# Performance work log

Measured on AMD Instinct MI355X. Metric: run time of the kernel, lower is better.

Reference implementation:

```python
import jax, jax.numpy as jnp
import numpy as np

FG_THR = 0.7
BG_THR = 0.3
NUM_PER_IMAGE = 256
NUM_POS_MAX = int(NUM_PER_IMAGE * 0.5)  # positive_ratio = 0.5
BBOX_W = (1.0, 1.0, 1.0, 1.0)
BETA = 1.0 / 9.0


def _permute(t, C):
    # N x (A*C) x H x W -> N x (H*W*A) x C, matching RPNLoss.permute
    N, _, H, W = t.shape
    t = t.reshape(N, -1, C, H, W)
    t = jnp.transpose(t, (0, 3, 4, 1, 2))
    return t.reshape(N, -1, C)


def _iou(a, b):
    # a: [N,4], b: [M,4] -> [N,M] (with +1 box convention, as in source)
    x_tl = jnp.maximum(a[:, None, 0], b[None, :, 0])
    y_tl = jnp.maximum(a[:, None, 1], b[None, :, 1])
    x_rb = jnp.minimum(a[:, None, 2], b[None, :, 2])
    y_rb = jnp.minimum(a[:, None, 3], b[None, :, 3])
    inter = jnp.clip(x_rb - x_tl + 1.0, 0.0) * jnp.clip(y_rb - y_tl + 1.0, 0.0)
    area1 = (a[:, 2] - a[:, 0] + 1.0) * (a[:, 3] - a[:, 1] + 1.0)
    area2 = (b[:, 2] - b[:, 0] + 1.0) * (b[:, 3] - b[:, 1] + 1.0)
    return inter / (area1[:, None] + area2[None, :] - inter)


def _encode(anchors, targets):
    ws = anchors[:, 2] - anchors[:, 0] + 1.0
    hs = anchors[:, 3] - anchors[:, 1] + 1.0
    x_ctr = anchors[:, 0] + 0.5 * ws
    y_ctr = anchors[:, 1] + 0.5 * hs
    t_ws = targets[:, 2] - targets[:, 0] + 1.0
    t_hs = targets[:, 3] - targets[:, 1] + 1.0
    t_x = targets[:, 0] + 0.5 * t_ws
    t_y = targets[:, 1] + 0.5 * t_hs
    wx, wy, ww, wh = BBOX_W
    tx = wx * (t_x - x_ctr) / ws
    ty = wy * (t_y - y_ctr) / hs
    tw = ww * jnp.log(t_ws / ws)
    th = wh * jnp.log(t_hs / hs)
    return jnp.stack([tx, ty, tw, th], axis=1)


def _bce_logits(l, t):
    return jnp.maximum(l, 0.0) - l * t + jnp.log1p(jnp.exp(-jnp.abs(l)))


def _per_image(anchor, logit, breg, size, target, key):
    N = anchor.shape[0]
    ious = _iou(anchor, target)  # [N, M]
    vals = ious.max(axis=1)
    ori = jnp.argmax(ious, axis=1).astype(jnp.int32)
    inds = jnp.where(vals < BG_THR, -1, ori)
    inds = jnp.where((vals >= BG_THR) & (vals < FG_THR), -2, inds)
    # low-quality matches: anchors achieving the per-target max IoU keep their argmax
    col_max = ious.max(axis=0)
    restore = (ious == col_max[None, :]).any(axis=1)
    inds = jnp.where(restore, ori, inds)
    # filter_anchors: keep anchors fully inside the image (size = (h, w))
    inside = (anchor[:, 0] >= 0) & (anchor[:, 1] >= 0) & \
             (anchor[:, 2] <= size[1] - 1.0) & (anchor[:, 3] <= size[0] - 1.0)
    inds = jnp.where(inside, inds, -2)

    pos = inds >= 0
    neg = inds == -1
    # random sampling via random priorities + fixed-size top_k with validity masks
    r = jax.random.uniform(key, (N,))
    pos_vals, pos_idx = jax.lax.top_k(jnp.where(pos, r, -1.0), NUM_POS_MAX)
    valid_pos = pos_vals >= 0.0
    num_pos = valid_pos.sum()
    neg_vals, neg_idx = jax.lax.top_k(jnp.where(neg, r, -1.0), NUM_PER_IMAGE)
    valid_neg = (neg_vals >= 0.0) & (jnp.arange(NUM_PER_IMAGE) < (NUM_PER_IMAGE - num_pos))

    # classification loss terms (BCE with logits); pos target 1, neg target 0
    vp = valid_pos.astype(logit.dtype)
    vn = valid_neg.astype(logit.dtype)
    cls_sum = jnp.sum(_bce_logits(logit[pos_idx], 1.0) * vp) + \
              jnp.sum(_bce_logits(logit[neg_idx], 0.0) * vn)
    count = num_pos + valid_neg.sum()

    m = jnp.clip(inds[pos_idx], 0, None)
    offsets = _encode(anchor[pos_idx], target[m])
    diff = jnp.abs(breg[pos_idx] - offsets)
    sl1 = jnp.where(diff < BETA, 0.5 * diff * diff / BETA, diff - 0.5 * BETA)
    reg_sum = jnp.sum(sl1 * vp[:, None])
    return cls_sum, count, reg_sum


def reference(anchors, logits, bbox_regs, sizes, targets):
    B = anchors.shape[0]
    log = _permute(logits, 1)[..., 0]      # [B, H*W*A]
    breg = _permute(bbox_regs, 4)          # [B, H*W*A, 4]
    keys = jax.random.split(jax.random.key(42), B)
    cls_s, cnt, reg_s = jax.vmap(_per_image)(anchors, log, breg, sizes, targets, keys)
    total = jnp.sum(cnt).astype(anchors.dtype)
    cls_loss = jnp.sum(cls_s) / total
    reg_loss = jnp.sum(reg_s) / total
    return jnp.stack([cls_loss, reg_loss])


def setup_inputs() -> dict:
    key = jax.random.key(0)
    ks = jax.random.split(key, 10)
    B, A, H, W, M = 4, 3, 168, 256, 32
    N = H * W * A
    IMG_H, IMG_W = 800.0, 1333.0
    x1 = jax.random.uniform(ks[0], (B, N)) * 1200.0
    y1 = jax.random.uniform(ks[1], (B, N)) * 700.0
    aw = jax.random.uniform(ks[2], (B, N)) * 300.0 + 16.0
    ah = jax.random.uniform(ks[3], (B, N)) * 300.0 + 16.0
    anchors = jnp.stack([x1, y1, x1 + aw, y1 + ah], axis=-1)  # some out of image -> filtered
    tx1 = jax.random.uniform(ks[4], (B, M)) * 1000.0
    ty1 = jax.random.uniform(ks[5], (B, M)) * 500.0
    tw = jax.random.uniform(ks[6], (B, M)) * 250.0 + 30.0
    th = jax.random.uniform(ks[7], (B, M)) * 200.0 + 30.0
    targets = jnp.stack([tx1, ty1, jnp.minimum(tx1 + tw, IMG_W - 1.0),
                         jnp.minimum(ty1 + th, IMG_H - 1.0)], axis=-1)
    logits = jax.random.normal(ks[8], (B, A, H, W), dtype=jnp.float32)
    bbox_regs = jax.random.normal(ks[9], (B, 4 * A, H, W), dtype=jnp.float32) * 0.1
    sizes = jnp.tile(jnp.array([IMG_H, IMG_W], dtype=jnp.float32), (B, 1))
    return {"anchors": anchors, "logits": logits, "bbox_regs": bbox_regs,
            "sizes": sizes, "targets": targets}
```

## Files before the change

### kernel.cpp

```cpp
#include <hip/hip_runtime.h>
#include <stdint.h>

#define Bn 4
#define An 3
#define Hn 168
#define Wn 256
#define Mn 32
#define HWn (Hn*Wn)
#define Nn (HWn*An)
#define POS_CAP 8192
#define NPERIM 256
#define NPOSMAX 128
#define FG_THR 0.7f
#define BG_THR 0.3f
#define BETA (1.0f/9.0f)

#define NBLK 504
#define APT 1
#define NWAVES (NBLK * 4)
#define BUCKET_CAP 256
#define TSEG_CAP 64

#define OFF_POSCNT 0
#define OFF_COUNT  8
#define OFF_CLS    9
#define OFF_REG    10
#define OFF_DONE   11
#define OFF_BINCNT 16
#define OFF_BINBCE 4112
#define ZERO_WORDS 8208
#define OFF_PCM    8208
#define OFF_WPCM   72720
#define OFF_TSEGC  330768
#define OFF_PLIST  338832
#define OFF_BUCKET 404368
#define OFF_TSEG   2501520

__device__ __forceinline__ uint32_t rotl32(uint32_t v, int n) { return (v << n) | (v >> (32 - n)); }

__device__ __forceinline__ void tf2x32(uint32_t k0, uint32_t k1, uint32_t x0, uint32_t x1,
                                       uint32_t& o0, uint32_t& o1) {
    uint32_t k2 = k0 ^ k1 ^ 0x1BD11BDAu;
    x0 += k0; x1 += k1;
    x0 += x1; x1 = rotl32(x1, 13); x1 ^= x0;
    x0 += x1; x1 = rotl32(x1, 15); x1 ^= x0;
    x0 += x1; x1 = rotl32(x1, 26); x1 ^= x0;
    x0 += x1; x1 = rotl32(x1, 6);  x1 ^= x0;
    x0 += k1; x1 += k2 + 1u;
    x0 += x1; x1 = rotl32(x1, 17); x1 ^= x0;
    x0 += x1; x1 = rotl32(x1, 29); x1 ^= x0;
    x0 += x1; x1 = rotl32(x1, 16); x1 ^= x0;
    x0 += x1; x1 = rotl32(x1, 24); x1 ^= x0;
    x0 += k2; x1 += k0 + 2u;
    x0 += x1; x1 = rotl32(x1, 13); x1 ^= x0;
    x0 += x1; x1 = rotl32(x1, 15); x1 ^= x0;
    x0 += x1; x1 = rotl32(x1, 26); x1 ^= x0;
    x0 += x1; x1 = rotl32(x1, 6);  x1 ^= x0;
    x0 += k0; x1 += k1 + 3u;
    x0 += x1; x1 = rotl32(x1, 17); x1 ^= x0;
    x0 += x1; x1 = rotl32(x1, 29); x1 ^= x0;
    x0 += x1; x1 = rotl32(x1, 16); x1 ^= x0;
    x0 += x1; x1 = rotl32(x1, 24); x1 ^= x0;
    x0 += k1; x1 += k2 + 4u;
    x0 += x1; x1 = rotl32(x1, 13); x1 ^= x0;
    x0 += x1; x1 = rotl32(x1, 15); x1 ^= x0;
    x0 += x1; x1 = rotl32(x1, 26); x1 ^= x0;
    x0 += x1; x1 = rotl32(x1, 6);  x1 ^= x0;
    x0 += k2; x1 += k0 + 5u;
    o0 = x0; o1 = x1;
}

__device__ __forceinline__ uint32_t rng_m23(uint32_t k0, uint32_t k1, uint32_t i) {
    uint32_t o0, o1;
    tf2x32(k0, k1, 0u, i, o0, o1);
    return (o0 ^ o1) >> 9;
}

__device__ __forceinline__ uint32_t vload(const uint32_t* p) {
    return *(const volatile uint32_t*)p;
}

__device__ __forceinline__ float iou_one(float a0, float a1, float a2, float a3,
                                         float t0, float t1, float t2, float t3) {
    float xtl = fmaxf(a0, t0), ytl = fmaxf(a1, t1);
    float xrb = fminf(a2, t2), yrb = fminf(a3, t3);
    float iw = fmaxf(xrb - xtl + 1.0f, 0.0f);
    float ih = fmaxf(yrb - ytl + 1.0f, 0.0f);
    float inter = iw * ih;
    float area1 = (a2 - a0 + 1.0f) * (a3 - a1 + 1.0f);
    float area2 = (t2 - t0 + 1.0f) * (t3 - t1 + 1.0f);
    return inter * __builtin_amdgcn_rcpf(area1 + area2 - inter);
}

__device__ __forceinline__ float bce0(float l) {
    return fmaxf(l, 0.0f) + log1pf(expf(-fabsf(l)));
}

__device__ __forceinline__ bool sel_less(uint2 a, uint2 b) {
    return (a.x > b.x) || (a.x == b.x && a.y < b.y);
}

__device__ void bitonic_sort_shared(uint2* buf, int n) {
    for (int k = 2; k <= n; k <<= 1) {
        for (int j = k >> 1; j > 0; j >>= 1) {
            for (int t = (int)threadIdx.x; t < n; t += (int)blockDim.x) {
                int ixj = t ^ j;
                if (ixj > t) {
                    uint2 x = buf[t], y = buf[ixj];
                    bool up = ((t & k) == 0);
                    bool sw = up ? sel_less(y, x) : sel_less(x, y);
                    if (sw) { buf[t] = y; buf[ixj] = x; }
                }
            }
            __syncthreads();
        }
    }
}

__global__ void __launch_bounds__(256) k0_init(uint32_t* __restrict__ ws) {
    int i = blockIdx.x * 256 + (int)threadIdx.x;
    if (i < ZERO_WORDS) ws[i] = 0u;
}

__global__ void __launch_bounds__(256) k1_iou(const float* __restrict__ anchors,
                                              const float* __restrict__ targets,
                                              const float* __restrict__ sizes,
                                              const float* __restrict__ logits,
                                              uint32_t* __restrict__ ws) {
    const int b = blockIdx.y, j = blockIdx.x, tid = threadIdx.x;
    const int wid = tid >> 6, lane = tid & 63;
    __shared__ float part[4][Mn];

    uint32_t key0, key1;
    tf2x32(0u, 42u, 0u, (uint32_t)b, key0, key1);

    const int i = j * 256 + tid;
    float4 av = ((const float4*)anchors)[b * Nn + i];

    float rowmax = -1.0f; int ori = 0; uint32_t tie = 0u;
    float mycm = 0.0f;
    #pragma unroll 4
    for (int t = 0; t < Mn; ++t) {
        float4 tv = ((const float4*)targets)[b * Mn + t];
        float io = iou_one(av.x, av.y, av.z, av.w, tv.x, tv.y, tv.z, tv.w);
        if (io > rowmax) { rowmax = io; ori = t; }
        float m0 = io;
        #pragma unroll
        for (int o = 32; o > 0; o >>= 1) m0 = fmaxf(m0, __shfl_xor(m0, o, 64));
        if (lane == t) mycm = m0;
        tie |= (io == m0) ? (1u << t) : 0u;
    }

    const int wimg = j * 4 + wid;
    if (lane < Mn) {
        ws[OFF_WPCM + ((size_t)b * NWAVES + wimg) * 32 + lane] = __float_as_uint(mycm);
        part[wid][lane] = mycm;
    }
    __syncthreads();
    if (tid < Mn) {
        float v = fmaxf(fmaxf(part[0][tid], part[1][tid]),
                        fmaxf(part[2][tid], part[3][tid]));
        ws[OFF_PCM + ((size_t)b * NBLK + j) * Mn + tid] = __float_as_uint(v);
    }

    const float sh = sizes[b * 2 + 0], sw = sizes[b * 2 + 1];
    unsigned long long lt_mask = (lane == 63) ? 0x7FFFFFFFFFFFFFFFull
                                              : ((1ull << lane) - 1ull);
    bool inside = (av.x >= 0.0f) && (av.y >= 0.0f) &&
                  (av.z <= sw - 1.0f) && (av.w <= sh - 1.0f);
    bool fg = rowmax >= FG_THR;
    bool bg = rowmax < BG_THR;
    bool posn   = inside && fg;
    bool defern = inside && !fg && (tie != 0u);
    bool negn   = inside && bg && (tie == 0u);
    uint32_t m = rng_m23(key0, key1, (uint32_t)i);

    const int a_ = i % An, hw_ = i / An;
    float lneg = 0.0f;
    if (negn) lneg = logits[(b * An + a_) * HWn + hw_];

    unsigned long long pmask = __ballot(posn);
    if (pmask) {
        int leader = __ffsll((long long)pmask) - 1;
        uint32_t bb = 0;
        if (lane == leader) bb = atomicAdd(&ws[OFF_POSCNT + b], (uint32_t)__popcll(pmask));
        bb = __shfl(bb, leader, 64);
        if (posn) {
            uint32_t p = bb + (uint32_t)__popcll(pmask & lt_mask);
            if (p < POS_CAP)
                ((uint2*)(ws + OFF_PLIST))[(size_t)b * POS_CAP + p] =
                    make_uint2(m, (uint32_t)i | ((uint32_t)ori << 17));
        }
    }
    unsigned long long dmask = __ballot(defern);
    if (defern) {
        uint32_t slot = (uint32_t)__popcll(dmask & lt_mask);
        ((uint4*)(ws + OFF_TSEG))[((size_t)b * NWAVES + wimg) * TSEG_CAP + slot] =
            make_uint4(tie, m,
                       (uint32_t)i | ((uint32_t)ori << 17) | (bg ? (1u << 22) : 0u),
                       0u);
    }
    if (lane == 0) ws[OFF_TSEGC + b * NWAVES + wimg] = (uint32_t)__popcll(dmask);
    if (negn) {
        int bin = (int)(m >> 13);
        uint32_t slot = atomicAdd(&ws[OFF_BINCNT + (b << 10) + bin], 1u);
        if (slot < BUCKET_CAP)
            ((uint2*)(ws + OFF_BUCKET))[((((size_t)b << 10) + bin) << 8) + slot] =
                make_uint2(m, (uint32_t)i);
        atomicAdd((float*)&ws[OFF_BINBCE + (b << 10) + bin], bce0(lneg));
    }
}

__global__ void __launch_bounds__(256) k2_resolve(const float* __restrict__ logits,
                                                  uint32_t* __restrict__ ws) {
    const int b = blockIdx.y, j = blockIdx.x, tid = threadIdx.x;
    const int lane = tid & 63;
    __shared__ float redf[256];
    __shared__ uint32_t cmb[Mn];
    __shared__ uint32_t eqs[4];
    __shared__ uint32_t cnts[4];

    {
        int t = tid & 31, sub = tid >> 5;
        float acc = 0.0f;
        for (int jj = sub; jj < NBLK; jj += 8)
            acc = fmaxf(acc, __uint_as_float(ws[OFF_PCM + ((size_t)b * NBLK + jj) * Mn + t]));
        redf[tid] = acc;
        __syncthreads();
        if (sub == 0) {
            #pragma unroll
            for (int q = 1; q < 8; ++q) acc = fmaxf(acc, redf[t + 32 * q]);
            cmb[t] = __float_as_uint(acc);
        }
    }
    if (tid < 4) {
        eqs[tid] = 0u;
        cnts[tid] = ws[OFF_TSEGC + b * NWAVES + j * 4 + tid];
    }
    __syncthreads();
    if (tid < 128) {
        int lw = tid >> 5, t2 = tid & 31;
        uint32_t wv = ws[OFF_WPCM + ((size_t)b * NWAVES + j * 4 + lw) * 32 + t2];
        if (wv == cmb[t2]) atomicOr(&eqs[lw], 1u << t2);
    }
    __syncthreads();

    const uint32_t c0 = cnts[0], c1 = cnts[1], c2 = cnts[2], c3 = cnts[3];
    const int total = (int)(c0 + c1 + c2 + c3);
    unsigned long long lt_mask = (lane == 63) ? 0x7FFFFFFFFFFFFFFFull
                                              : ((1ull << lane) - 1ull);
    for (int f = tid; f < total; f += 256) {
        int lw, o;
        if ((uint32_t)f < c0)                { lw = 0; o = f; }
        else if ((uint32_t)f < c0 + c1)      { lw = 1; o = f - (int)c0; }
        else if ((uint32_t)f < c0 + c1 + c2) { lw = 2; o = f - (int)(c0 + c1); }
        else                                 { lw = 3; o = f - (int)(c0 + c1 + c2); }
        uint4 e = ((const uint4*)(ws + OFF_TSEG))
                      [((size_t)b * NWAVES + j * 4 + lw) * TSEG_CAP + o];
        int i = (int)(e.z & 0x1FFFFu);
        bool restored = (e.x & eqs[lw]) != 0u;

        unsigned long long rmask = __ballot(restored);
        if (rmask) {
            int leader = __ffsll((long long)rmask) - 1;
            uint32_t bb = 0;
            if (lane == leader) bb = atomicAdd(&ws[OFF_POSCNT + b], (uint32_t)__popcll(rmask));
            bb = __shfl(bb, leader, 64);
            if (restored) {
                uint32_t p = bb + (uint32_t)__popcll(rmask & lt_mask);
                if (p < POS_CAP)
                    ((uint2*)(ws + OFF_PLIST))[(size_t)b * POS_CAP + p] =
                        make_uint2(e.y, e.z & 0x3FFFFFu);
            }
        }
        if (!restored && (e.z & (1u << 22))) {
            uint32_t m = e.y;
            int bin = (int)(m >> 13);
            uint32_t slot = atomicAdd(&ws[OFF_BINCNT + (b << 10) + bin], 1u);
            if (slot < BUCKET_CAP)
                ((uint2*)(ws + OFF_BUCKET))[((((size_t)b << 10) + bin) << 8) + slot] =
                    make_uint2(m, (uint32_t)i);
            int a = i % An, hw = i / An;
            float l = logits[(b * An + a) * HWn + hw];
            atomicAdd((float*)&ws[OFF_BINBCE + (b << 10) + bin], bce0(l));
        }
    }
}

__global__ void __launch_bounds__(1024) k3_final(const float* __restrict__ anchors,
                                                 const float* __restrict__ targets,
                                                 const float* __restrict__ logits,
                                                 const float* __restrict__ bregs,
                                                 uint32_t* __restrict__ ws,
                                                 float* __restrict__ out) {
    const int b = blockIdx.x, tid = threadIdx.x;
    __shared__ uint32_t csum[1024];
    __shared__ uint2 buf[2048];
    __shared__ float fred[1024];
    __shared__ int s_bd, s_need;
    float cls = 0.0f, reg = 0.0f;

    csum[tid] = vload(ws + OFF_BINCNT + (b << 10) + tid);
    __syncthreads();
    for (int off = 1; off < 1024; off <<= 1) {
        uint32_t v = csum[tid];
        uint32_t add = (tid + off < 1024) ? csum[tid + off] : 0u;
        __syncthreads();
        csum[tid] = v + add;
        __syncthreads();
    }
    uint32_t pc = vload(ws + OFF_POSCNT + b);
    int num_pos = (pc < (uint32_t)NPOSMAX) ? (int)pc : NPOSMAX;
    int k_neg = NPERIM - num_pos;
    uint32_t total = csum[0];
    if (tid == 0 && (int)total < k_neg) { s_bd = -1; s_need = 0; }
    {
        uint32_t inclv = csum[tid];
        uint32_t nxt = (tid < 1023) ? csum[tid + 1] : 0u;
        if ((int)total >= k_neg && (int)inclv >= k_neg && (int)nxt < k_neg) {
            s_bd = tid; s_need = k_neg - (int)nxt;
        }
    }
    if (tid == 0) {
        int sel_negs = ((int)total < k_neg) ? (int)total : k_neg;
        atomicAdd(&ws[OFF_COUNT], (uint32_t)(num_pos + sel_negs));
    }
    __syncthreads();
    const int bd = s_bd, need = s_need;
    if ((int)tid > bd)
        cls += __uint_as_float(vload(ws + OFF_BINBCE + (b << 10) + tid));
    __syncthreads();

    if (need > 0) {
        int cnt = (int)vload(ws + OFF_BINCNT + (b << 10) + bd);
        if (cnt > BUCKET_CAP) cnt = BUCKET_CAP;
        const uint2* bkt = (const uint2*)(ws + OFF_BUCKET) + ((((size_t)b << 10) + bd) << 8);
        for (int t = tid; t < cnt; t += 1024) buf[t] = bkt[t];
        int npad = 1; while (npad < cnt) npad <<= 1;
        for (int t = tid; t < npad; t += 1024) if (t >= cnt) buf[t] = make_uint2(0u, 0xFFFFFFFFu);
        __syncthreads();
        bitonic_sort_shared(buf, npad);
        int sel = (need < cnt) ? need : cnt;
        for (int t = tid; t < sel; t += 1024) {
            int i = (int)buf[t].y;
            int a = i % An, hw = i / An;
            float l = logits[(b * An + a) * HWn + hw];
            cls += bce0(l);
        }
    }
    __syncthreads();

    {
        int pci = (pc < (uint32_t)POS_CAP) ? (int)pc : POS_CAP;
        const uint2* plist = (const uint2*)(ws + OFF_PLIST) + (size_t)b * POS_CAP;
        int psel = (pci < NPOSMAX) ? pci : NPOSMAX;
        bool use_buf = false;
        if (pci > NPOSMAX) {
            int n = (pci < 2048) ? pci : 2048;
            for (int t = tid; t < n; t += 1024) buf[t] = plist[t];
            int npad = 1; while (npad < n) npad <<= 1;
            for (int t = tid; t < npad; t += 1024) if (t >= n) buf[t] = make_uint2(0u, 0xFFFFFFFFu);
            __syncthreads();
            bitonic_sort_shared(buf, npad);
            use_buf = true;
            psel = (NPOSMAX < n) ? NPOSMAX : n;
        }
        for (int t = tid; t < psel; t += 1024) {
            uint32_t packed = use_buf ? buf[t].y : plist[t].y;
            int i = (int)(packed & 0x1FFFFu);
            int orit = (int)((packed >> 17) & 0x1Fu);
            int a = i % An, hw = i / An;
            float l = logits[(b * An + a) * HWn + hw];
            cls += fmaxf(l, 0.0f) - l + log1pf(expf(-fabsf(l)));
            float4 avx = ((const float4*)anchors)[b * Nn + i];
            float4 tv = ((const float4*)targets)[b * Mn + orit];
            float aws = avx.z - avx.x + 1.0f, ahs = avx.w - avx.y + 1.0f;
            float axc = avx.x + 0.5f * aws, ayc = avx.y + 0.5f * ahs;
            float tws = tv.z - tv.x + 1.0f, ths = tv.w - tv.y + 1.0f;
            float txc = tv.x + 0.5f * tws, tyc = tv.y + 0.5f * ths;
            float off0 = (txc - axc) / aws;
            float off1 = (tyc - ayc) / ahs;
            float off2 = logf(tws / aws);
            float off3 = logf(ths / ahs);
            float br0 = bregs[(b * 12 + a * 4 + 0) * HWn + hw];
            float br1 = bregs[(b * 12 + a * 4 + 1) * HWn + hw];
            float br2 = bregs[(b * 12 + a * 4 + 2) * HWn + hw];
            float br3 = bregs[(b * 12 + a * 4 + 3) * HWn + hw];
            float d;
            d = fabsf(br0 - off0); reg += (d < BETA) ? 0.5f * d * d / BETA : d - 0.5f * BETA;
            d = fabsf(br1 - off1); reg += (d < BETA) ? 0.5f * d * d / BETA : d - 0.5f * BETA;
            d = fabsf(br2 - off2); reg += (d < BETA) ? 0.5f * d * d / BETA : d - 0.5f * BETA;
            d = fabsf(br3 - off3); reg += (d < BETA) ? 0.5f * d * d / BETA : d - 0.5f * BETA;
        }
    }

    fred[tid] = cls;
    __syncthreads();
    for (int s = 512; s > 0; s >>= 1) {
        if (tid < s) fred[tid] += fred[tid + s];
        __syncthreads();
    }
    if (tid == 0 && fred[0] != 0.0f) atomicAdd((float*)&ws[OFF_CLS], fred[0]);
    __syncthreads();
    fred[tid] = reg;
    __syncthreads();
    for (int s = 512; s > 0; s >>= 1) {
        if (tid < s) fred[tid] += fred[tid + s];
        __syncthreads();
    }
    if (tid == 0) {
        if (fred[0] != 0.0f) atomicAdd((float*)&ws[OFF_REG], fred[0]);
        __threadfence();
        uint32_t old = atomicAdd(&ws[OFF_DONE], 1u);
        if (old == Bn - 1) {
            float cls_tot = __uint_as_float(atomicAdd(&ws[OFF_CLS], 0u));
            float reg_tot = __uint_as_float(atomicAdd(&ws[OFF_REG], 0u));
            float cnt = (float)atomicAdd(&ws[OFF_COUNT], 0u);
            out[0] = cls_tot / cnt;
            out[1] = reg_tot / cnt;
        }
    }
}

extern "C" void kernel_launch(void* const* d_in, const int* in_sizes, int n_in,
                              void* d_out, int out_size, void* d_ws, size_t ws_size,
                              hipStream_t stream) {
    const float* anchors = (const float*)d_in[0];
    const float* logits  = (const float*)d_in[1];
    const float* bregs   = (const float*)d_in[2];
    const float* sizes   = (const float*)d_in[3];
    const float* targets = (const float*)d_in[4];
    float* out = (float*)d_out;
    uint32_t* ws = (uint32_t*)d_ws;

    k0_init<<<dim3((ZERO_WORDS + 255) / 256), dim3(256), 0, stream>>>(ws);
    k1_iou<<<dim3(NBLK, Bn), dim3(256), 0, stream>>>(anchors, targets, sizes, logits, ws);
    k2_resolve<<<dim3(NBLK, Bn), dim3(256), 0, stream>>>(logits, ws);
    k3_final<<<dim3(Bn), dim3(1024), 0, stream>>>(anchors, targets, logits, bregs, ws, out);
}
```

Baseline: 190.2 us.

## Fuse final selection into resolve kernel via last-block pattern and per-wave negative segments

The final per-image selection kernel is merged into the resolve kernel: the last block to finish for each image, detected with an atomic counter, does the histogram scan, boundary-bin gather, sorts and loss sums. Negative candidates are now written to per-wave segments, and only high-score bins keep global buckets. Other boundary bins are rebuilt by scanning all segments in the finishing block. This removes one kernel launch and most per-negative bucket scatter writes. The cost is a possibly long serial scan over thousands of segments when the boundary bin is cold, and the tail work runs on a 256-thread block instead of 1024.

```diff
diff --git a/kernel.cpp b/kernel.cpp
--- a/kernel.cpp
+++ b/kernel.cpp
@@ -16,25 +16,33 @@
 #define BETA (1.0f/9.0f)
 
 #define NBLK 504
-#define APT 1
-#define NWAVES (NBLK * 4)
-#define BUCKET_CAP 256
+#define NWAVES (NBLK*4)
 #define TSEG_CAP 64
+#define NSEG_CAP 64
+#define XSEG_CAP 256
+#define BIN_HOT 960
+#define NHOT 64
+#define HB_CAP 256
 
 #define OFF_POSCNT 0
+#define OFF_DONEI  4
 #define OFF_COUNT  8
 #define OFF_CLS    9
 #define OFF_REG    10
-#define OFF_DONE   11
+#define OFF_DONEA  11
 #define OFF_BINCNT 16
 #define OFF_BINBCE 4112
 #define ZERO_WORDS 8208
 #define OFF_PCM    8208
 #define OFF_WPCM   72720
 #define OFF_TSEGC  330768
-#define OFF_PLIST  338832
-#define OFF_BUCKET 404368
-#define OFF_TSEG   2501520
+#define OFF_NSEGC  338832
+#define OFF_XSEGC  346896
+#define OFF_PLIST  348912
+#define OFF_HBUCK  414448
+#define OFF_TSEG   545520
+#define OFF_NSEG   2609904
+#define OFF_XSEG   3642096
 
 __device__ __forceinline__ uint32_t rotl32(uint32_t v, int n) { return (v << n) | (v >> (32 - n)); }
 
@@ -80,6 +88,11 @@
     return *(const volatile uint32_t*)p;
 }
 
+__device__ __forceinline__ void st64(uint2* p, uint2 v) {
+    atomicExch((unsigned long long*)p,
+               ((unsigned long long)v.y << 32) | (unsigned long long)v.x);
+}
+
 __device__ __forceinline__ float iou_one(float a0, float a1, float a2, float a3,
                                          float t0, float t1, float t2, float t3) {
     float xtl = fmaxf(a0, t0), ytl = fmaxf(a1, t1);
@@ -197,152 +210,231 @@
         uint32_t slot = (uint32_t)__popcll(dmask & lt_mask);
         ((uint4*)(ws + OFF_TSEG))[((size_t)b * NWAVES + wimg) * TSEG_CAP + slot] =
             make_uint4(tie, m,
-                       (uint32_t)i | ((uint32_t)ori << 17) | (bg ? (1u << 22) : 0u),
-                       0u);
-    }
-    if (lane == 0) ws[OFF_TSEGC + b * NWAVES + wimg] = (uint32_t)__popcll(dmask);
+                       (uint32_t)i | ((uint32_t)ori << 17) | (bg ? (1u << 22) : 0u), 0u);
+    }
+    unsigned long long nmask = __ballot(negn);
     if (negn) {
+        uint32_t slot = (uint32_t)__popcll(nmask & lt_mask);
+        ((uint2*)(ws + OFF_NSEG))[((size_t)b * NWAVES + wimg) * NSEG_CAP + slot] =
+            make_uint2(m, (uint32_t)i);
         int bin = (int)(m >> 13);
-        uint32_t slot = atomicAdd(&ws[OFF_BINCNT + (b << 10) + bin], 1u);
-        if (slot < BUCKET_CAP)
-            ((uint2*)(ws + OFF_BUCKET))[((((size_t)b << 10) + bin) << 8) + slot] =
-                make_uint2(m, (uint32_t)i);
+        if (bin >= BIN_HOT) {
+            uint32_t s2 = atomicAdd(&ws[OFF_BINCNT + (b << 10) + bin], 1u);
+            if (s2 < HB_CAP)
+                ((uint2*)(ws + OFF_HBUCK))[((size_t)b * NHOT + (bin - BIN_HOT)) * HB_CAP + s2] =
+                    make_uint2(m, (uint32_t)i);
+        } else {
+            atomicAdd(&ws[OFF_BINCNT + (b << 10) + bin], 1u);
+        }
         atomicAdd((float*)&ws[OFF_BINBCE + (b << 10) + bin], bce0(lneg));
     }
-}
-
-__global__ void __launch_bounds__(256) k2_resolve(const float* __restrict__ logits,
-                                                  uint32_t* __restrict__ ws) {
+    if (lane == 0) {
+        ws[OFF_TSEGC + b * NWAVES + wimg] = (uint32_t)__popcll(dmask);
+        ws[OFF_NSEGC + b * NWAVES + wimg] = (uint32_t)__popcll(nmask);
+    }
+}
+
+__global__ void __launch_bounds__(256) k2_resolve(const float* __restrict__ anchors,
+                                                  const float* __restrict__ targets,
+                                                  const float* __restrict__ logits,
+                                                  const float* __restrict__ bregs,
+                                                  uint32_t* __restrict__ ws,
+                                                  float* __restrict__ out) {
     const int b = blockIdx.y, j = blockIdx.x, tid = threadIdx.x;
     const int lane = tid & 63;
-    __shared__ float redf[256];
     __shared__ uint32_t cmb[Mn];
     __shared__ uint32_t eqs[4];
     __shared__ uint32_t cnts[4];
-
-    {
-        int t = tid & 31, sub = tid >> 5;
-        float acc = 0.0f;
-        for (int jj = sub; jj < NBLK; jj += 8)
-            acc = fmaxf(acc, __uint_as_float(ws[OFF_PCM + ((size_t)b * NBLK + jj) * Mn + t]));
-        redf[tid] = acc;
+    __shared__ uint32_t sx_cnt, s_fcnt;
+    __shared__ int s_last, s_bd, s_need;
+    union U {
+        float part[8][32];
+        struct { uint32_t csum[256]; uint2 buf[2048]; float red[256]; } fin;
+    };
+    __shared__ U u;
+
+    if (tid < 4) { eqs[tid] = 0u; cnts[tid] = ws[OFF_TSEGC + b * NWAVES + j * 4 + tid]; }
+    if (tid == 0) sx_cnt = 0u;
+    __syncthreads();
+    const int total = (int)(cnts[0] + cnts[1] + cnts[2] + cnts[3]);
+
+    if (total > 0) {
+        {
+            float acc = 0.0f;
+            const uint32_t* pcm = ws + OFF_PCM + (size_t)b * NBLK * Mn;
+            for (int w = tid; w < NBLK * Mn; w += 256)
+                acc = fmaxf(acc, __uint_as_float(pcm[w]));
+            u.part[tid >> 5][tid & 31] = acc;
+            __syncthreads();
+            if (tid < Mn) {
+                float v = u.part[0][tid];
+                #pragma unroll
+                for (int q = 1; q < 8; ++q) v = fmaxf(v, u.part[q][tid]);
+                cmb[tid] = __float_as_uint(v);
+            }
+            __syncthreads();
+        }
+        if (tid < 128) {
+            int lw = tid >> 5, t2 = tid & 31;
+            uint32_t wv = ws[OFF_WPCM + ((size_t)b * NWAVES + j * 4 + lw) * 32 + t2];
+            if (wv == cmb[t2]) atomicOr(&eqs[lw], 1u << t2);
+        }
         __syncthreads();
-        if (sub == 0) {
-            #pragma unroll
-            for (int q = 1; q < 8; ++q) acc = fmaxf(acc, redf[t + 32 * q]);
-            cmb[t] = __float_as_uint(acc);
-        }
-    }
-    if (tid < 4) {
-        eqs[tid] = 0u;
-        cnts[tid] = ws[OFF_TSEGC + b * NWAVES + j * 4 + tid];
-    }
-    __syncthreads();
-    if (tid < 128) {
-        int lw = tid >> 5, t2 = tid & 31;
-        uint32_t wv = ws[OFF_WPCM + ((size_t)b * NWAVES + j * 4 + lw) * 32 + t2];
-        if (wv == cmb[t2]) atomicOr(&eqs[lw], 1u << t2);
-    }
-    __syncthreads();
-
-    const uint32_t c0 = cnts[0], c1 = cnts[1], c2 = cnts[2], c3 = cnts[3];
-    const int total = (int)(c0 + c1 + c2 + c3);
-    unsigned long long lt_mask = (lane == 63) ? 0x7FFFFFFFFFFFFFFFull
-                                              : ((1ull << lane) - 1ull);
-    for (int f = tid; f < total; f += 256) {
-        int lw, o;
-        if ((uint32_t)f < c0)                { lw = 0; o = f; }
-        else if ((uint32_t)f < c0 + c1)      { lw = 1; o = f - (int)c0; }
-        else if ((uint32_t)f < c0 + c1 + c2) { lw = 2; o = f - (int)(c0 + c1); }
-        else                                 { lw = 3; o = f - (int)(c0 + c1 + c2); }
-        uint4 e = ((const uint4*)(ws + OFF_TSEG))
-                      [((size_t)b * NWAVES + j * 4 + lw) * TSEG_CAP + o];
-        int i = (int)(e.z & 0x1FFFFu);
-        bool restored = (e.x & eqs[lw]) != 0u;
-
-        unsigned long long rmask = __ballot(restored);
-        if (rmask) {
-            int leader = __ffsll((long long)rmask) - 1;
-            uint32_t bb = 0;
-            if (lane == leader) bb = atomicAdd(&ws[OFF_POSCNT + b], (uint32_t)__popcll(rmask));
-            bb = __shfl(bb, leader, 64);
-            if (restored) {
-                uint32_t p = bb + (uint32_t)__popcll(rmask & lt_mask);
-                if (p < POS_CAP)
-                    ((uint2*)(ws + OFF_PLIST))[(size_t)b * POS_CAP + p] =
-                        make_uint2(e.y, e.z & 0x3FFFFFu);
-            }
-        }
-        if (!restored && (e.z & (1u << 22))) {
-            uint32_t m = e.y;
-            int bin = (int)(m >> 13);
-            uint32_t slot = atomicAdd(&ws[OFF_BINCNT + (b << 10) + bin], 1u);
-            if (slot < BUCKET_CAP)
-                ((uint2*)(ws + OFF_BUCKET))[((((size_t)b << 10) + bin) << 8) + slot] =
-                    make_uint2(m, (uint32_t)i);
-            int a = i % An, hw = i / An;
-            float l = logits[(b * An + a) * HWn + hw];
-            atomicAdd((float*)&ws[OFF_BINBCE + (b << 10) + bin], bce0(l));
-        }
-    }
-}
-
-__global__ void __launch_bounds__(1024) k3_final(const float* __restrict__ anchors,
-                                                 const float* __restrict__ targets,
-                                                 const float* __restrict__ logits,
-                                                 const float* __restrict__ bregs,
-                                                 uint32_t* __restrict__ ws,
-                                                 float* __restrict__ out) {
-    const int b = blockIdx.x, tid = threadIdx.x;
-    __shared__ uint32_t csum[1024];
-    __shared__ uint2 buf[2048];
-    __shared__ float fred[1024];
-    __shared__ int s_bd, s_need;
+
+        const uint32_t c0 = cnts[0], c1 = cnts[1], c2 = cnts[2], c3 = cnts[3];
+        unsigned long long lt_mask = (lane == 63) ? 0x7FFFFFFFFFFFFFFFull
+                                                  : ((1ull << lane) - 1ull);
+        for (int f = tid; f < total; f += 256) {
+            int lw, o;
+            if ((uint32_t)f < c0)                { lw = 0; o = f; }
+            else if ((uint32_t)f < c0 + c1)      { lw = 1; o = f - (int)c0; }
+            else if ((uint32_t)f < c0 + c1 + c2) { lw = 2; o = f - (int)(c0 + c1); }
+            else                                 { lw = 3; o = f - (int)(c0 + c1 + c2); }
+            uint4 e = ((const uint4*)(ws + OFF_TSEG))
+                          [((size_t)b * NWAVES + j * 4 + lw) * TSEG_CAP + o];
+            int i = (int)(e.z & 0x1FFFFu);
+            bool restored = (e.x & eqs[lw]) != 0u;
+
+            unsigned long long rmask = __ballot(restored);
+            if (rmask) {
+                int leader = __ffsll((long long)rmask) - 1;
+                uint32_t bb = 0;
+                if (lane == leader) bb = atomicAdd(&ws[OFF_POSCNT + b], (uint32_t)__popcll(rmask));
+                bb = __shfl(bb, leader, 64);
+                if (restored) {
+                    uint32_t p = bb + (uint32_t)__popcll(rmask & lt_mask);
+                    if (p < POS_CAP)
+                        st64(&((uint2*)(ws + OFF_PLIST))[(size_t)b * POS_CAP + p],
+                             make_uint2(e.y, e.z & 0x3FFFFFu));
+                }
+            }
+            if (!restored && (e.z & (1u << 22))) {
+                uint32_t m = e.y;
+                int bin = (int)(m >> 13);
+                if (bin >= BIN_HOT) {
+                    uint32_t s2 = atomicAdd(&ws[OFF_BINCNT + (b << 10) + bin], 1u);
+                    if (s2 < HB_CAP)
+                        st64(&((uint2*)(ws + OFF_HBUCK))
+                                 [((size_t)b * NHOT + (bin - BIN_HOT)) * HB_CAP + s2],
+                             make_uint2(m, (uint32_t)i));
+                } else {
+                    atomicAdd(&ws[OFF_BINCNT + (b << 10) + bin], 1u);
+                }
+                int a = i % An, hw = i / An;
+                float l = logits[(b * An + a) * HWn + hw];
+                atomicAdd((float*)&ws[OFF_BINBCE + (b << 10) + bin], bce0(l));
+                uint32_t xs = atomicAdd(&sx_cnt, 1u);
+                if (xs < XSEG_CAP)
+                    st64(&((uint2*)(ws + OFF_XSEG))[((size_t)b * NBLK + j) * XSEG_CAP + xs],
+                         make_uint2(m, (uint32_t)i));
+            }
+        }
+    }
+    __syncthreads();
+    if (tid == 0) ws[OFF_XSEGC + b * NBLK + j] = sx_cnt;
+
+    __threadfence();
+    __syncthreads();
+    if (tid == 0) {
+        uint32_t old = atomicAdd(&ws[OFF_DONEI + b], 1u);
+        s_last = (old == (uint32_t)(NBLK - 1)) ? 1 : 0;
+    }
+    __syncthreads();
+    if (!s_last) return;
+
+    __threadfence();
     float cls = 0.0f, reg = 0.0f;
 
-    csum[tid] = vload(ws + OFF_BINCNT + (b << 10) + tid);
-    __syncthreads();
-    for (int off = 1; off < 1024; off <<= 1) {
-        uint32_t v = csum[tid];
-        uint32_t add = (tid + off < 1024) ? csum[tid + off] : 0u;
+    uint32_t c4[4];
+    #pragma unroll
+    for (int q = 0; q < 4; ++q) c4[q] = vload(ws + OFF_BINCNT + (b << 10) + 4 * tid + q);
+    u.fin.csum[tid] = c4[0] + c4[1] + c4[2] + c4[3];
+    __syncthreads();
+    for (int off = 1; off < 256; off <<= 1) {
+        uint32_t mine = u.fin.csum[tid];
+        uint32_t add = (tid + off < 256) ? u.fin.csum[tid + off] : 0u;
         __syncthreads();
-        csum[tid] = v + add;
+        u.fin.csum[tid] = mine + add;
         __syncthreads();
     }
     uint32_t pc = vload(ws + OFF_POSCNT + b);
     int num_pos = (pc < (uint32_t)NPOSMAX) ? (int)pc : NPOSMAX;
     int k_neg = NPERIM - num_pos;
-    uint32_t total = csum[0];
-    if (tid == 0 && (int)total < k_neg) { s_bd = -1; s_need = 0; }
+    uint32_t total_n = u.fin.csum[0];
+    if (tid == 0 && (int)total_n < k_neg) { s_bd = -1; s_need = 0; }
     {
-        uint32_t inclv = csum[tid];
-        uint32_t nxt = (tid < 1023) ? csum[tid + 1] : 0u;
-        if ((int)total >= k_neg && (int)inclv >= k_neg && (int)nxt < k_neg) {
-            s_bd = tid; s_need = k_neg - (int)nxt;
+        uint32_t incl = u.fin.csum[tid];
+        uint32_t nxt = (tid < 255) ? u.fin.csum[tid + 1] : 0u;
+        if ((int)total_n >= k_neg && (int)incl >= k_neg && (int)nxt < k_neg) {
+            int cum = (int)nxt, boundary = -1, needed = 0;
+            #pragma unroll
+            for (int q = 3; q >= 0; --q) {
+                int c = (int)c4[q];
+                if (cum + c >= k_neg) { boundary = 4 * tid + q; needed = k_neg - cum; break; }
+                cum += c;
+            }
+            s_bd = boundary; s_need = needed;
         }
     }
     if (tid == 0) {
-        int sel_negs = ((int)total < k_neg) ? (int)total : k_neg;
+        int sel_negs = ((int)total_n < k_neg) ? (int)total_n : k_neg;
         atomicAdd(&ws[OFF_COUNT], (uint32_t)(num_pos + sel_negs));
     }
     __syncthreads();
     const int bd = s_bd, need = s_need;
-    if ((int)tid > bd)
-        cls += __uint_as_float(vload(ws + OFF_BINBCE + (b << 10) + tid));
+    #pragma unroll
+    for (int q = 0; q < 4; ++q) {
+        int bin = 4 * tid + q;
+        if (bin > bd) cls += __uint_as_float(vload(ws + OFF_BINBCE + (b << 10) + bin));
+    }
     __syncthreads();
 
     if (need > 0) {
-        int cnt = (int)vload(ws + OFF_BINCNT + (b << 10) + bd);
-        if (cnt > BUCKET_CAP) cnt = BUCKET_CAP;
-        const uint2* bkt = (const uint2*)(ws + OFF_BUCKET) + ((((size_t)b << 10) + bd) << 8);
-        for (int t = tid; t < cnt; t += 1024) buf[t] = bkt[t];
+        int cnt;
+        if (bd >= BIN_HOT) {
+            cnt = (int)vload(ws + OFF_BINCNT + (b << 10) + bd);
+            if (cnt > HB_CAP) cnt = HB_CAP;
+            const uint2* bkt = (const uint2*)(ws + OFF_HBUCK) +
+                               ((size_t)b * NHOT + (bd - BIN_HOT)) * HB_CAP;
+            for (int t = tid; t < cnt; t += 256) u.fin.buf[t] = bkt[t];
+        } else {
+            if (tid == 0) s_fcnt = 0u;
+            __syncthreads();
+            for (int w = 0; w < NWAVES; ++w) {
+                int cw = (int)vload(ws + OFF_NSEGC + b * NWAVES + w);
+                const uint2* ns = (const uint2*)(ws + OFF_NSEG) +
+                                  ((size_t)b * NWAVES + w) * NSEG_CAP;
+                for (int idx = tid; idx < cw; idx += 256) {
+                    uint2 e = ns[idx];
+                    if ((int)(e.x >> 13) == bd) {
+                        uint32_t q2 = atomicAdd(&s_fcnt, 1u);
+                        if (q2 < 2048u) u.fin.buf[q2] = e;
+                    }
+                }
+            }
+            for (int j2 = 0; j2 < NBLK; ++j2) {
+                int cx = (int)vload(ws + OFF_XSEGC + b * NBLK + j2);
+                if (cx > XSEG_CAP) cx = XSEG_CAP;
+                const uint2* xs = (const uint2*)(ws + OFF_XSEG) +
+                                  ((size_t)b * NBLK + j2) * XSEG_CAP;
+                for (int idx = tid; idx < cx; idx += 256) {
+                    uint2 e = xs[idx];
+                    if ((int)(e.x >> 13) == bd) {
+                        uint32_t q2 = atomicAdd(&s_fcnt, 1u);
+                        if (q2 < 2048u) u.fin.buf[q2] = e;
+                    }
+                }
+            }
+            __syncthreads();
+            cnt = (int)s_fcnt; if (cnt > 2048) cnt = 2048;
+        }
         int npad = 1; while (npad < cnt) npad <<= 1;
-        for (int t = tid; t < npad; t += 1024) if (t >= cnt) buf[t] = make_uint2(0u, 0xFFFFFFFFu);
+        for (int t = tid; t < npad; t += 256) if (t >= cnt) u.fin.buf[t] = make_uint2(0u, 0xFFFFFFFFu);
         __syncthreads();
-        bitonic_sort_shared(buf, npad);
+        bitonic_sort_shared(u.fin.buf, npad);
         int sel = (need < cnt) ? need : cnt;
-        for (int t = tid; t < sel; t += 1024) {
-            int i = (int)buf[t].y;
+        for (int t = tid; t < sel; t += 256) {
+            int i = (int)u.fin.buf[t].y;
             int a = i % An, hw = i / An;
             float l = logits[(b * An + a) * HWn + hw];
             cls += bce0(l);
@@ -357,16 +449,16 @@
         bool use_buf = false;
         if (pci > NPOSMAX) {
             int n = (pci < 2048) ? pci : 2048;
-            for (int t = tid; t < n; t += 1024) buf[t] = plist[t];
+            for (int t = tid; t < n; t += 256) u.fin.buf[t] = plist[t];
             int npad = 1; while (npad < n) npad <<= 1;
-            for (int t = tid; t < npad; t += 1024) if (t >= n) buf[t] = make_uint2(0u, 0xFFFFFFFFu);
+            for (int t = tid; t < npad; t += 256) if (t >= n) u.fin.buf[t] = make_uint2(0u, 0xFFFFFFFFu);
             __syncthreads();
-            bitonic_sort_shared(buf, npad);
+            bitonic_sort_shared(u.fin.buf, npad);
             use_buf = true;
             psel = (NPOSMAX < n) ? NPOSMAX : n;
         }
-        for (int t = tid; t < psel; t += 1024) {
-            uint32_t packed = use_buf ? buf[t].y : plist[t].y;
+        for (int t = tid; t < psel; t += 256) {
+            uint32_t packed = use_buf ? u.fin.buf[t].y : plist[t].y;
             int i = (int)(packed & 0x1FFFFu);
             int orit = (int)((packed >> 17) & 0x1Fu);
             int a = i % An, hw = i / An;
@@ -393,25 +485,26 @@
             d = fabsf(br3 - off3); reg += (d < BETA) ? 0.5f * d * d / BETA : d - 0.5f * BETA;
         }
     }
-
-    fred[tid] = cls;
-    __syncthreads();
-    for (int s = 512; s > 0; s >>= 1) {
-        if (tid < s) fred[tid] += fred[tid + s];
+    __syncthreads();
+
+    u.fin.red[tid] = cls;
+    __syncthreads();
+    for (int s = 128; s > 0; s >>= 1) {
+        if (tid < s) u.fin.red[tid] += u.fin.red[tid + s];
         __syncthreads();
     }
-    if (tid == 0 && fred[0] != 0.0f) atomicAdd((float*)&ws[OFF_CLS], fred[0]);
-    __syncthreads();
-    fred[tid] = reg;
-    __syncthreads();
-    for (int s = 512; s > 0; s >>= 1) {
-        if (tid < s) fred[tid] += fred[tid + s];
+    if (tid == 0 && u.fin.red[0] != 0.0f) atomicAdd((float*)&ws[OFF_CLS], u.fin.red[0]);
+    __syncthreads();
+    u.fin.red[tid] = reg;
+    __syncthreads();
+    for (int s = 128; s > 0; s >>= 1) {
+        if (tid < s) u.fin.red[tid] += u.fin.red[tid + s];
         __syncthreads();
     }
     if (tid == 0) {
-        if (fred[0] != 0.0f) atomicAdd((float*)&ws[OFF_REG], fred[0]);
+        if (u.fin.red[0] != 0.0f) atomicAdd((float*)&ws[OFF_REG], u.fin.red[0]);
         __threadfence();
-        uint32_t old = atomicAdd(&ws[OFF_DONE], 1u);
+        uint32_t old = atomicAdd(&ws[OFF_DONEA], 1u);
         if (old == Bn - 1) {
             float cls_tot = __uint_as_float(atomicAdd(&ws[OFF_CLS], 0u));
             float reg_tot = __uint_as_float(atomicAdd(&ws[OFF_REG], 0u));
@@ -435,6 +528,5 @@
 
     k0_init<<<dim3((ZERO_WORDS + 255) / 256), dim3(256), 0, stream>>>(ws);
     k1_iou<<<dim3(NBLK, Bn), dim3(256), 0, stream>>>(anchors, targets, sizes, logits, ws);
-    k2_resolve<<<dim3(NBLK, Bn), dim3(256), 0, stream>>>(logits, ws);
-    k3_final<<<dim3(Bn), dim3(1024), 0, stream>>>(anchors, targets, logits, bregs, ws, out);
-}
+    k2_resolve<<<dim3(NBLK, Bn), dim3(256), 0, stream>>>(anchors, targets, logits, bregs, ws, out);
+}
```

New measurement: 307.0 us. 61.4% more time.

## Replace per-block column-max partials with atomicMax and bucket only hot bins

Applied to the files above, without the earlier changes.

Per-target column max is now reduced with a global atomicMax into padded slots, so k2 no longer has to re-reduce 504 partials per block. Negative candidates are written to per-wave segments, and only the high-score bins (bin >= 960) get global buckets. If the boundary bin is a cold one, k3 rebuilds its contents by scanning those segments. Resolve blocks with no deferred entries skip their work early. This cuts k2 redundant reads and bucket writes, at the cost of contended atomics on 32 addresses per image and a possibly long scan in k3 on the rare path.

```diff
diff --git a/kernel.cpp b/kernel.cpp
--- a/kernel.cpp
+++ b/kernel.cpp
@@ -16,25 +16,33 @@
 #define BETA (1.0f/9.0f)
 
 #define NBLK 504
-#define APT 1
-#define NWAVES (NBLK * 4)
-#define BUCKET_CAP 256
+#define NWAVES (NBLK*4)
 #define TSEG_CAP 64
+#define NSEG_CAP 64
+#define XSEG_CAP 256
+#define BIN_HOT 960
+#define NHOT 64
+#define HB_CAP 256
+#define CM_STRIDE 16
 
 #define OFF_POSCNT 0
 #define OFF_COUNT  8
 #define OFF_CLS    9
 #define OFF_REG    10
-#define OFF_DONE   11
+#define OFF_DONEA  11
 #define OFF_BINCNT 16
 #define OFF_BINBCE 4112
-#define ZERO_WORDS 8208
-#define OFF_PCM    8208
-#define OFF_WPCM   72720
-#define OFF_TSEGC  330768
-#define OFF_PLIST  338832
-#define OFF_BUCKET 404368
-#define OFF_TSEG   2501520
+#define OFF_CM     8208
+#define ZERO_WORDS 10256
+#define OFF_WPCM   10256
+#define OFF_TSEGC  268304
+#define OFF_NSEGC  276368
+#define OFF_XSEGC  284432
+#define OFF_PLIST  286448
+#define OFF_HBUCK  351984
+#define OFF_TSEG   483056
+#define OFF_NSEG   2547440
+#define OFF_XSEG   3579632
 
 __device__ __forceinline__ uint32_t rotl32(uint32_t v, int n) { return (v << n) | (v >> (32 - n)); }
 
@@ -76,10 +84,6 @@
     return (o0 ^ o1) >> 9;
 }
 
-__device__ __forceinline__ uint32_t vload(const uint32_t* p) {
-    return *(const volatile uint32_t*)p;
-}
-
 __device__ __forceinline__ float iou_one(float a0, float a1, float a2, float a3,
                                          float t0, float t1, float t2, float t3) {
     float xtl = fmaxf(a0, t0), ytl = fmaxf(a1, t1);
@@ -160,7 +164,7 @@
     if (tid < Mn) {
         float v = fmaxf(fmaxf(part[0][tid], part[1][tid]),
                         fmaxf(part[2][tid], part[3][tid]));
-        ws[OFF_PCM + ((size_t)b * NBLK + j) * Mn + tid] = __float_as_uint(v);
+        atomicMax(&ws[OFF_CM + (b * 32 + tid) * CM_STRIDE], __float_as_uint(v));
     }
 
     const float sh = sizes[b * 2 + 0], sw = sizes[b * 2 + 1];
@@ -197,17 +201,27 @@
         uint32_t slot = (uint32_t)__popcll(dmask & lt_mask);
         ((uint4*)(ws + OFF_TSEG))[((size_t)b * NWAVES + wimg) * TSEG_CAP + slot] =
             make_uint4(tie, m,
-                       (uint32_t)i | ((uint32_t)ori << 17) | (bg ? (1u << 22) : 0u),
-                       0u);
-    }
-    if (lane == 0) ws[OFF_TSEGC + b * NWAVES + wimg] = (uint32_t)__popcll(dmask);
+                       (uint32_t)i | ((uint32_t)ori << 17) | (bg ? (1u << 22) : 0u), 0u);
+    }
+    unsigned long long nmask = __ballot(negn);
     if (negn) {
+        uint32_t slot = (uint32_t)__popcll(nmask & lt_mask);
+        ((uint2*)(ws + OFF_NSEG))[((size_t)b * NWAVES + wimg) * NSEG_CAP + slot] =
+            make_uint2(m, (uint32_t)i);
         int bin = (int)(m >> 13);
-        uint32_t slot = atomicAdd(&ws[OFF_BINCNT + (b << 10) + bin], 1u);
-        if (slot < BUCKET_CAP)
-            ((uint2*)(ws + OFF_BUCKET))[((((size_t)b << 10) + bin) << 8) + slot] =
-                make_uint2(m, (uint32_t)i);
+        if (bin >= BIN_HOT) {
+            uint32_t s2 = atomicAdd(&ws[OFF_BINCNT + (b << 10) + bin], 1u);
+            if (s2 < HB_CAP)
+                ((uint2*)(ws + OFF_HBUCK))[((size_t)b * NHOT + (bin - BIN_HOT)) * HB_CAP + s2] =
+                    make_uint2(m, (uint32_t)i);
+        } else {
+            atomicAdd(&ws[OFF_BINCNT + (b << 10) + bin], 1u);
+        }
         atomicAdd((float*)&ws[OFF_BINBCE + (b << 10) + bin], bce0(lneg));
+    }
+    if (lane == 0) {
+        ws[OFF_TSEGC + b * NWAVES + wimg] = (uint32_t)__popcll(dmask);
+        ws[OFF_NSEGC + b * NWAVES + wimg] = (uint32_t)__popcll(nmask);
     }
 }
 
@@ -215,76 +229,75 @@
                                                   uint32_t* __restrict__ ws) {
     const int b = blockIdx.y, j = blockIdx.x, tid = threadIdx.x;
     const int lane = tid & 63;
-    __shared__ float redf[256];
     __shared__ uint32_t cmb[Mn];
     __shared__ uint32_t eqs[4];
     __shared__ uint32_t cnts[4];
-
-    {
-        int t = tid & 31, sub = tid >> 5;
-        float acc = 0.0f;
-        for (int jj = sub; jj < NBLK; jj += 8)
-            acc = fmaxf(acc, __uint_as_float(ws[OFF_PCM + ((size_t)b * NBLK + jj) * Mn + t]));
-        redf[tid] = acc;
-        __syncthreads();
-        if (sub == 0) {
-            #pragma unroll
-            for (int q = 1; q < 8; ++q) acc = fmaxf(acc, redf[t + 32 * q]);
-            cmb[t] = __float_as_uint(acc);
-        }
-    }
-    if (tid < 4) {
-        eqs[tid] = 0u;
-        cnts[tid] = ws[OFF_TSEGC + b * NWAVES + j * 4 + tid];
-    }
-    __syncthreads();
-    if (tid < 128) {
-        int lw = tid >> 5, t2 = tid & 31;
-        uint32_t wv = ws[OFF_WPCM + ((size_t)b * NWAVES + j * 4 + lw) * 32 + t2];
-        if (wv == cmb[t2]) atomicOr(&eqs[lw], 1u << t2);
-    }
-    __syncthreads();
-
-    const uint32_t c0 = cnts[0], c1 = cnts[1], c2 = cnts[2], c3 = cnts[3];
-    const int total = (int)(c0 + c1 + c2 + c3);
-    unsigned long long lt_mask = (lane == 63) ? 0x7FFFFFFFFFFFFFFFull
-                                              : ((1ull << lane) - 1ull);
-    for (int f = tid; f < total; f += 256) {
-        int lw, o;
-        if ((uint32_t)f < c0)                { lw = 0; o = f; }
-        else if ((uint32_t)f < c0 + c1)      { lw = 1; o = f - (int)c0; }
-        else if ((uint32_t)f < c0 + c1 + c2) { lw = 2; o = f - (int)(c0 + c1); }
-        else                                 { lw = 3; o = f - (int)(c0 + c1 + c2); }
-        uint4 e = ((const uint4*)(ws + OFF_TSEG))
-                      [((size_t)b * NWAVES + j * 4 + lw) * TSEG_CAP + o];
-        int i = (int)(e.z & 0x1FFFFu);
-        bool restored = (e.x & eqs[lw]) != 0u;
-
-        unsigned long long rmask = __ballot(restored);
-        if (rmask) {
-            int leader = __ffsll((long long)rmask) - 1;
-            uint32_t bb = 0;
-            if (lane == leader) bb = atomicAdd(&ws[OFF_POSCNT + b], (uint32_t)__popcll(rmask));
-            bb = __shfl(bb, leader, 64);
-            if (restored) {
-                uint32_t p = bb + (uint32_t)__popcll(rmask & lt_mask);
-                if (p < POS_CAP)
-                    ((uint2*)(ws + OFF_PLIST))[(size_t)b * POS_CAP + p] =
-                        make_uint2(e.y, e.z & 0x3FFFFFu);
+    __shared__ uint32_t sx_cnt;
+
+    if (tid < 4) { eqs[tid] = 0u; cnts[tid] = ws[OFF_TSEGC + b * NWAVES + j * 4 + tid]; }
+    if (tid == 0) sx_cnt = 0u;
+    if (tid < Mn) cmb[tid] = ws[OFF_CM + (b * 32 + tid) * CM_STRIDE];
+    __syncthreads();
+    const int total = (int)(cnts[0] + cnts[1] + cnts[2] + cnts[3]);
+    if (total > 0) {
+        if (tid < 128) {
+            int lw = tid >> 5, t2 = tid & 31;
+            uint32_t wv = ws[OFF_WPCM + ((size_t)b * NWAVES + j * 4 + lw) * 32 + t2];
+            if (wv == cmb[t2]) atomicOr(&eqs[lw], 1u << t2);
+        }
+        __syncthreads();
+
+        const uint32_t c0 = cnts[0], c1 = cnts[1], c2 = cnts[2], c3 = cnts[3];
+        unsigned long long lt_mask = (lane == 63) ? 0x7FFFFFFFFFFFFFFFull
+                                                  : ((1ull << lane) - 1ull);
+        for (int f = tid; f < total; f += 256) {
+            int lw, o;
+            if ((uint32_t)f < c0)                { lw = 0; o = f; }
+            else if ((uint32_t)f < c0 + c1)      { lw = 1; o = f - (int)c0; }
+            else if ((uint32_t)f < c0 + c1 + c2) { lw = 2; o = f - (int)(c0 + c1); }
+            else                                 { lw = 3; o = f - (int)(c0 + c1 + c2); }
+            uint4 e = ((const uint4*)(ws + OFF_TSEG))
+                          [((size_t)b * NWAVES + j * 4 + lw) * TSEG_CAP + o];
+            int i = (int)(e.z & 0x1FFFFu);
+            bool restored = (e.x & eqs[lw]) != 0u;
+
+            unsigned long long rmask = __ballot(restored);
+            if (rmask) {
+                int leader = __ffsll((long long)rmask) - 1;
+                uint32_t bb = 0;
+                if (lane == leader) bb = atomicAdd(&ws[OFF_POSCNT + b], (uint32_t)__popcll(rmask));
+                bb = __shfl(bb, leader, 64);
+                if (restored) {
+                    uint32_t p = bb + (uint32_t)__popcll(rmask & lt_mask);
+                    if (p < POS_CAP)
+                        ((uint2*)(ws + OFF_PLIST))[(size_t)b * POS_CAP + p] =
+                            make_uint2(e.y, e.z & 0x3FFFFFu);
+                }
             }
-        }
-        if (!restored && (e.z & (1u << 22))) {
-            uint32_t m = e.y;
-            int bin = (int)(m >> 13);
-            uint32_t slot = atomicAdd(&ws[OFF_BINCNT + (b << 10) + bin], 1u);
-            if (slot < BUCKET_CAP)
-                ((uint2*)(ws + OFF_BUCKET))[((((size_t)b << 10) + bin) << 8) + slot] =
-                    make_uint2(m, (uint32_t)i);
-            int a = i % An, hw = i / An;
-            float l = logits[(b * An + a) * HWn + hw];
-            atomicAdd((float*)&ws[OFF_BINBCE + (b << 10) + bin], bce0(l));
-        }
-    }
+            if (!restored && (e.z & (1u << 22))) {
+                uint32_t m = e.y;
+                int bin = (int)(m >> 13);
+                if (bin >= BIN_HOT) {
+                    uint32_t s2 = atomicAdd(&ws[OFF_BINCNT + (b << 10) + bin], 1u);
+                    if (s2 < HB_CAP)
+                        ((uint2*)(ws + OFF_HBUCK))
+                            [((size_t)b * NHOT + (bin - BIN_HOT)) * HB_CAP + s2] =
+                                make_uint2(m, (uint32_t)i);
+                } else {
+                    atomicAdd(&ws[OFF_BINCNT + (b << 10) + bin], 1u);
+                }
+                int a = i % An, hw = i / An;
+                float l = logits[(b * An + a) * HWn + hw];
+                atomicAdd((float*)&ws[OFF_BINBCE + (b << 10) + bin], bce0(l));
+                uint32_t xs = atomicAdd(&sx_cnt, 1u);
+                if (xs < XSEG_CAP)
+                    ((uint2*)(ws + OFF_XSEG))[((size_t)b * NBLK + j) * XSEG_CAP + xs] =
+                        make_uint2(m, (uint32_t)i);
+            }
+        }
+    }
+    __syncthreads();
+    if (tid == 0) ws[OFF_XSEGC + b * NBLK + j] = sx_cnt;
 }
 
 __global__ void __launch_bounds__(1024) k3_final(const float* __restrict__ anchors,
@@ -298,9 +311,10 @@
     __shared__ uint2 buf[2048];
     __shared__ float fred[1024];
     __shared__ int s_bd, s_need;
+    __shared__ uint32_t s_fcnt;
     float cls = 0.0f, reg = 0.0f;
 
-    csum[tid] = vload(ws + OFF_BINCNT + (b << 10) + tid);
+    csum[tid] = ws[OFF_BINCNT + (b << 10) + tid];
     __syncthreads();
     for (int off = 1; off < 1024; off <<= 1) {
         uint32_t v = csum[tid];
@@ -309,7 +323,7 @@
         csum[tid] = v + add;
         __syncthreads();
     }
-    uint32_t pc = vload(ws + OFF_POSCNT + b);
+    uint32_t pc = ws[OFF_POSCNT + b];
     int num_pos = (pc < (uint32_t)NPOSMAX) ? (int)pc : NPOSMAX;
     int k_neg = NPERIM - num_pos;
     uint32_t total = csum[0];
@@ -328,14 +342,48 @@
     __syncthreads();
     const int bd = s_bd, need = s_need;
     if ((int)tid > bd)
-        cls += __uint_as_float(vload(ws + OFF_BINBCE + (b << 10) + tid));
+        cls += __uint_as_float(ws[OFF_BINBCE + (b << 10) + tid]);
     __syncthreads();
 
     if (need > 0) {
-        int cnt = (int)vload(ws + OFF_BINCNT + (b << 10) + bd);
-        if (cnt > BUCKET_CAP) cnt = BUCKET_CAP;
-        const uint2* bkt = (const uint2*)(ws + OFF_BUCKET) + ((((size_t)b << 10) + bd) << 8);
-        for (int t = tid; t < cnt; t += 1024) buf[t] = bkt[t];
+        int cnt;
+        if (bd >= BIN_HOT) {
+            cnt = (int)ws[OFF_BINCNT + (b << 10) + bd];
+            if (cnt > HB_CAP) cnt = HB_CAP;
+            const uint2* bkt = (const uint2*)(ws + OFF_HBUCK) +
+                               ((size_t)b * NHOT + (bd - BIN_HOT)) * HB_CAP;
+            for (int t = tid; t < cnt; t += 1024) buf[t] = bkt[t];
+        } else {
+            if (tid == 0) s_fcnt = 0u;
+            __syncthreads();
+            for (int w = tid >> 6; w < NWAVES; w += 16) {
+                int cw = (int)ws[OFF_NSEGC + b * NWAVES + w];
+                const uint2* ns = (const uint2*)(ws + OFF_NSEG) +
+                                  ((size_t)b * NWAVES + w) * NSEG_CAP;
+                for (int idx = (tid & 63); idx < cw; idx += 64) {
+                    uint2 e = ns[idx];
+                    if ((int)(e.x >> 13) == bd) {
+                        uint32_t q2 = atomicAdd(&s_fcnt, 1u);
+                        if (q2 < 2048u) buf[q2] = e;
+                    }
+                }
+            }
+            for (int j2 = tid >> 6; j2 < NBLK; j2 += 16) {
+                int cx = (int)ws[OFF_XSEGC + b * NBLK + j2];
+                if (cx > XSEG_CAP) cx = XSEG_CAP;
+                const uint2* xs = (const uint2*)(ws + OFF_XSEG) +
+                                  ((size_t)b * NBLK + j2) * XSEG_CAP;
+                for (int idx = (tid & 63); idx < cx; idx += 64) {
+                    uint2 e = xs[idx];
+                    if ((int)(e.x >> 13) == bd) {
+                        uint32_t q2 = atomicAdd(&s_fcnt, 1u);
+                        if (q2 < 2048u) buf[q2] = e;
+                    }
+                }
+            }
+            __syncthreads();
+            cnt = (int)s_fcnt; if (cnt > 2048) cnt = 2048;
+        }
         int npad = 1; while (npad < cnt) npad <<= 1;
         for (int t = tid; t < npad; t += 1024) if (t >= cnt) buf[t] = make_uint2(0u, 0xFFFFFFFFu);
         __syncthreads();
@@ -411,7 +459,7 @@
     if (tid == 0) {
         if (fred[0] != 0.0f) atomicAdd((float*)&ws[OFF_REG], fred[0]);
         __threadfence();
-        uint32_t old = atomicAdd(&ws[OFF_DONE], 1u);
+        uint32_t old = atomicAdd(&ws[OFF_DONEA], 1u);
         if (old == Bn - 1) {
             float cls_tot = __uint_as_float(atomicAdd(&ws[OFF_CLS], 0u));
             float reg_tot = __uint_as_float(atomicAdd(&ws[OFF_REG], 0u));
```

After: 172.3 us. 1.1x faster.
